# Optimization experiments

Measured on AMD Instinct MI355X. Metric: run time of the kernel, lower is better.

Reference implementation:

```python
import jax, jax.numpy as jnp
import numpy as np

N_NODES = 50000


def gcn_conv(x, row, col, deg_inv_sqrt, W, b, num_nodes):
    # PyG GCNConv: h = x @ W; out[i] = sum_{(j->i)} norm_ji * h[j] + b
    # norm_ji = deg^{-1/2}[j] * deg^{-1/2}[i], with self-loops already in (row, col).
    h = x @ W  # [N, C_out]
    norm = deg_inv_sqrt[row] * deg_inv_sqrt[col]  # [E+N]
    msgs = h[row] * norm[:, None]  # gather + scale, [E+N, C_out]
    out = jax.ops.segment_sum(msgs, col, num_segments=num_nodes)
    return out + b


def setup_inputs() -> dict:
    key = jax.random.key(0)
    ks = jax.random.split(key, 8)
    n, e = N_NODES, 1600000
    c_in, c_hid, c_out = 128, 64, 32
    x = jax.random.normal(ks[0], (n, c_in), dtype=jnp.float32)
    edge_index = jax.random.randint(ks[1], (2, e), 0, n, dtype=jnp.int64)
    s1 = 1.0 / np.sqrt(c_in)
    s2 = 1.0 / np.sqrt(c_hid)
    W1 = jax.random.uniform(ks[2], (c_in, c_hid), jnp.float32, -s1, s1)
    b1 = jnp.zeros((c_hid,), jnp.float32)
    W2 = jax.random.uniform(ks[3], (c_hid, c_out), jnp.float32, -s2, s2)
    b2 = jnp.zeros((c_out,), jnp.float32)
    W3 = jax.random.uniform(ks[4], (c_hid, c_out), jnp.float32, -s2, s2)
    b3 = jnp.zeros((c_out,), jnp.float32)
    return {"x": x, "edge_index": edge_index, "W1": W1, "b1": b1,
            "W2": W2, "b2": b2, "W3": W3, "b3": b3}


def reference(x, edge_index, W1, b1, W2, b2, W3, b3):
    n = x.shape[0]
    # add self-loops (PyG GCNConv default add_self_loops=True)
    loop = jnp.arange(n, dtype=edge_index.dtype)
    row = jnp.concatenate([edge_index[0], loop])
    col = jnp.concatenate([edge_index[1], loop])
    # symmetric normalization: deg computed over target nodes (unit edge weights)
    deg = jax.ops.segment_sum(jnp.ones_like(col, dtype=x.dtype), col, num_segments=n)
    deg_inv_sqrt = jnp.where(deg > 0, jax.lax.rsqrt(jnp.maximum(deg, 1.0)), 0.0)
    h = jax.nn.relu(gcn_conv(x, row, col, deg_inv_sqrt, W1, b1, n))
    mu = gcn_conv(h, row, col, deg_inv_sqrt, W2, b2, n)
    logvar = gcn_conv(h, row, col, deg_inv_sqrt, W3, b3, n)
    return (mu, logvar)
```

## Files before the change

kernel.cpp:

```cpp
#include <hip/hip_runtime.h>


#define NBMAX 256
#define NT2 256
#define SLOT 128
#define CAPSH 14
#define CAP (1 << CAPSH)

__device__ __forceinline__ ushort f2bf(float x) {
    unsigned u = __float_as_uint(x);
    u = (u + 0x7FFFu + ((u >> 16) & 1u)) >> 16;
    return (ushort)u;
}
__device__ __forceinline__ float bflo(unsigned u) { return __uint_as_float(u << 16); }
__device__ __forceinline__ float bfhi(unsigned u) { return __uint_as_float(u & 0xFFFF0000u); }

__device__ __forceinline__ void acc8(float* a, uint4 x) {
    a[0] += bflo(x.x); a[1] += bfhi(x.x);
    a[2] += bflo(x.y); a[3] += bfhi(x.y);
    a[4] += bflo(x.z); a[5] += bfhi(x.z);
    a[6] += bflo(x.w); a[7] += bfhi(x.w);
}

__global__ __launch_bounds__(256) void k_tilesort(const int* __restrict__ row,
                                                  const int* __restrict__ col,
                                                  int* __restrict__ binbuf,
                                                  unsigned char* __restrict__ cnt,
                                                  int e, int chunk) {
    __shared__ int lh[NBMAX];
    int tile = blockIdx.x;
    int t0 = tile * chunk;
    int t1 = t0 + chunk < e ? t0 + chunk : e;
    for (int i = threadIdx.x; i < NBMAX; i += 256) lh[i] = 0;
    __syncthreads();
    for (int i = t0 + threadIdx.x; i < t1; i += 256) {
        int c = col[i];
        int b = c >> 8;
        int pos = atomicAdd(&lh[b], 1);
        if (pos < SLOT)
            binbuf[(((b << 8) + tile) << 7) + pos] = row[i] | ((c & 255) << 16);
    }
    __syncthreads();
    for (int b = threadIdx.x; b < NBMAX; b += 256) {
        int c = lh[b];
        cnt[(tile << 8) + b] = (unsigned char)(c < SLOT ? c : SLOT);
    }
}

__global__ __launch_bounds__(256) void k_build(const int* __restrict__ binbuf,
                                               const unsigned char* __restrict__ cnt,
                                               float* __restrict__ dis,
                                               int* __restrict__ rp2,
                                               ushort* __restrict__ csr, int n) {
    __shared__ int lcnt[256], s[256], cur[256];
    int b = blockIdx.x;
    int t = threadIdx.x;
    int myc = cnt[(t << 8) + b];
    int mybase = ((b << 8) + t) << 7;
    lcnt[t] = 0;
    __syncthreads();
    for (int i = 0; i < myc; ++i) {
        int p = binbuf[mybase + i];
        atomicAdd(&lcnt[(p >> 16) & 255], 1);
    }
    __syncthreads();
    int v = lcnt[t];
    s[t] = v;
    __syncthreads();
    for (int off = 1; off < 256; off <<= 1) {
        int u = (t >= off) ? s[t - off] : 0;
        __syncthreads();
        s[t] += u;
        __syncthreads();
    }
    int node0 = b << 8;
    int nloc = n - node0 < 256 ? n - node0 : 256;
    int lo = b << CAPSH;
    if (t < nloc) {
        int beg = lo + s[t] - v;
        rp2[2 * (node0 + t)] = beg;
        rp2[2 * (node0 + t) + 1] = beg + v;
        cur[t] = beg;
        dis[node0 + t] = rsqrtf((float)v + 1.0f);
    }
    __syncthreads();
    for (int i = 0; i < myc; ++i) {
        int p = binbuf[mybase + i];
        int pos = atomicAdd(&cur[(p >> 16) & 255], 1);
        csr[pos] = (ushort)(p & 0xffff);
    }
}

__global__ __launch_bounds__(256) void k_gemm1(const float* __restrict__ x,
                                               const float* __restrict__ W,
                                               const float* __restrict__ dis,
                                               ushort* __restrict__ hs1b, int n) {
    __shared__ float4 w4[32][64];
    __shared__ float4 xs[4][16][8];
    for (int i = threadIdx.x; i < 128 * 64; i += 256) {
        int k = i >> 6, c = i & 63;
        ((float*)&w4[k >> 2][c])[k & 3] = W[i];
    }
    int wid = threadIdx.x >> 6;
    int lane = threadIdx.x & 63;
    int r0 = blockIdx.x * 64 + wid * 16;
    const float4* x4 = (const float4*)x;
    float acc[16];
#pragma unroll
    for (int r = 0; r < 16; ++r) acc[r] = 0.f;
    __syncthreads();
#pragma unroll
    for (int st = 0; st < 4; ++st) {
#pragma unroll
        for (int j = 0; j < 2; ++j) {
            int idx = j * 64 + lane;
            int rr = r0 + (idx >> 3);
            if (rr >= n) rr = n - 1;
            xs[wid][idx >> 3][idx & 7] = x4[(size_t)rr * 32 + st * 8 + (idx & 7)];
        }
#pragma unroll 2
        for (int k4 = 0; k4 < 8; ++k4) {
            float4 wv = w4[st * 8 + k4][lane];
#pragma unroll
            for (int r = 0; r < 16; ++r) {
                float4 xv = xs[wid][r][k4];
                acc[r] = fmaf(xv.x, wv.x, acc[r]);
                acc[r] = fmaf(xv.y, wv.y, acc[r]);
                acc[r] = fmaf(xv.z, wv.z, acc[r]);
                acc[r] = fmaf(xv.w, wv.w, acc[r]);
            }
        }
    }
    ushort* hb = hs1b + (size_t)(lane >> 5) * n * 32 + (lane & 31);
#pragma unroll
    for (int r = 0; r < 16; ++r) {
        int rw = r0 + r;
        if (rw < n) hb[(size_t)rw * 32] = f2bf(dis[rw] * acc[r]);
    }
}

__global__ __launch_bounds__(256) void k_pull1(const int* __restrict__ rp2,
                                               const ushort* __restrict__ csr,
                                               const ushort* __restrict__ hs1b,
                                               const float* __restrict__ dis,
                                               const float* __restrict__ b1,
                                               ushort* __restrict__ hs2b, int n) {
    int xcd = blockIdx.x & 7;
    int sid = xcd >> 2;
    int idx = (blockIdx.x >> 3) * 4 + (xcd & 3);
    int node = idx * 64 + (threadIdx.x >> 2);
    int c4 = threadIdx.x & 3;
    if (node >= n) return;
    size_t slab = (size_t)sid * n * 32;
    const uint4* h4 = (const uint4*)(hs1b + slab);
    int2 be = ((const int2*)rp2)[node];
    float a[8], b[8];
    uint4 v = h4[(size_t)node * 4 + c4];
    a[0] = bflo(v.x); a[1] = bfhi(v.x); a[2] = bflo(v.y); a[3] = bfhi(v.y);
    a[4] = bflo(v.z); a[5] = bfhi(v.z); a[6] = bflo(v.w); a[7] = bfhi(v.w);
#pragma unroll
    for (int j = 0; j < 8; ++j) b[j] = 0.f;
    int k = be.x;
    for (; k + 8 <= be.y; k += 8) {
        uint4 v0 = h4[(size_t)csr[k] * 4 + c4];
        uint4 v1 = h4[(size_t)csr[k + 1] * 4 + c4];
        uint4 v2 = h4[(size_t)csr[k + 2] * 4 + c4];
        uint4 v3 = h4[(size_t)csr[k + 3] * 4 + c4];
        uint4 v4 = h4[(size_t)csr[k + 4] * 4 + c4];
        uint4 v5 = h4[(size_t)csr[k + 5] * 4 + c4];
        uint4 v6 = h4[(size_t)csr[k + 6] * 4 + c4];
        uint4 v7 = h4[(size_t)csr[k + 7] * 4 + c4];
        acc8(a, v0); acc8(b, v1); acc8(a, v2); acc8(b, v3);
        acc8(a, v4); acc8(b, v5); acc8(a, v6); acc8(b, v7);
    }
    if (k + 4 <= be.y) {
        uint4 v0 = h4[(size_t)csr[k] * 4 + c4];
        uint4 v1 = h4[(size_t)csr[k + 1] * 4 + c4];
        uint4 v2 = h4[(size_t)csr[k + 2] * 4 + c4];
        uint4 v3 = h4[(size_t)csr[k + 3] * 4 + c4];
        acc8(a, v0); acc8(b, v1); acc8(a, v2); acc8(b, v3);
        k += 4;
    }
    for (; k < be.y; ++k) acc8(a, h4[(size_t)csr[k] * 4 + c4]);
    float d = dis[node];
    const float* b1s = b1 + sid * 32;
    float4 bb0 = *(const float4*)(b1s + c4 * 8);
    float4 bb1 = *(const float4*)(b1s + c4 * 8 + 4);
    float bj[8] = {bb0.x, bb0.y, bb0.z, bb0.w, bb1.x, bb1.y, bb1.z, bb1.w};
    float o[8];
#pragma unroll
    for (int j = 0; j < 8; ++j) {
        float tt = fmaf(d, a[j] + b[j], bj[j]);
        o[j] = tt > 0.f ? d * tt : 0.f;
    }
    uint4 w;
    w.x = (unsigned)f2bf(o[0]) | ((unsigned)f2bf(o[1]) << 16);
    w.y = (unsigned)f2bf(o[2]) | ((unsigned)f2bf(o[3]) << 16);
    w.z = (unsigned)f2bf(o[4]) | ((unsigned)f2bf(o[5]) << 16);
    w.w = (unsigned)f2bf(o[6]) | ((unsigned)f2bf(o[7]) << 16);
    ((uint4*)(hs2b + slab))[(size_t)node * 4 + c4] = w;
}

__global__ __launch_bounds__(256) void k_pull2(const int* __restrict__ rp2,
                                               const ushort* __restrict__ csr,
                                               const ushort* __restrict__ hs2b,
                                               const float* __restrict__ dis,
                                               float* __restrict__ gagg, int n) {
    int xcd = blockIdx.x & 7;
    int sid = xcd >> 2;
    int idx = (blockIdx.x >> 3) * 4 + (xcd & 3);
    int node = idx * 64 + (threadIdx.x >> 2);
    int c4 = threadIdx.x & 3;
    if (node >= n) return;
    const uint4* h4 = (const uint4*)(hs2b + (size_t)sid * n * 32);
    int2 be = ((const int2*)rp2)[node];
    float a[8], b[8];
    uint4 v = h4[(size_t)node * 4 + c4];
    a[0] = bflo(v.x); a[1] = bfhi(v.x); a[2] = bflo(v.y); a[3] = bfhi(v.y);
    a[4] = bflo(v.z); a[5] = bfhi(v.z); a[6] = bflo(v.w); a[7] = bfhi(v.w);
#pragma unroll
    for (int j = 0; j < 8; ++j) b[j] = 0.f;
    int k = be.x;
    for (; k + 8 <= be.y; k += 8) {
        uint4 v0 = h4[(size_t)csr[k] * 4 + c4];
        uint4 v1 = h4[(size_t)csr[k + 1] * 4 + c4];
        uint4 v2 = h4[(size_t)csr[k + 2] * 4 + c4];
        uint4 v3 = h4[(size_t)csr[k + 3] * 4 + c4];
        uint4 v4 = h4[(size_t)csr[k + 4] * 4 + c4];
        uint4 v5 = h4[(size_t)csr[k + 5] * 4 + c4];
        uint4 v6 = h4[(size_t)csr[k + 6] * 4 + c4];
        uint4 v7 = h4[(size_t)csr[k + 7] * 4 + c4];
        acc8(a, v0); acc8(b, v1); acc8(a, v2); acc8(b, v3);
        acc8(a, v4); acc8(b, v5); acc8(a, v6); acc8(b, v7);
    }
    if (k + 4 <= be.y) {
        uint4 v0 = h4[(size_t)csr[k] * 4 + c4];
        uint4 v1 = h4[(size_t)csr[k + 1] * 4 + c4];
        uint4 v2 = h4[(size_t)csr[k + 2] * 4 + c4];
        uint4 v3 = h4[(size_t)csr[k + 3] * 4 + c4];
        acc8(a, v0); acc8(b, v1); acc8(a, v2); acc8(b, v3);
        k += 4;
    }
    for (; k < be.y; ++k) acc8(a, h4[(size_t)csr[k] * 4 + c4]);
    float d = dis[node];
    float* dst = gagg + (size_t)node * 64 + sid * 32 + c4 * 8;
    *(float4*)dst = make_float4(d * (a[0] + b[0]), d * (a[1] + b[1]),
                                d * (a[2] + b[2]), d * (a[3] + b[3]));
    *(float4*)(dst + 4) = make_float4(d * (a[4] + b[4]), d * (a[5] + b[5]),
                                      d * (a[6] + b[6]), d * (a[7] + b[7]));
}

__global__ __launch_bounds__(256) void k_gemm23(const float* __restrict__ g,
                                                const float* __restrict__ W2,
                                                const float* __restrict__ b2,
                                                const float* __restrict__ W3,
                                                const float* __restrict__ b3,
                                                float* __restrict__ out, int n) {
    __shared__ float ws[2 * 32 * 17 * 4];
    __shared__ float4 gs[4][16 * 16];
    for (int i = threadIdx.x; i < 64 * 32; i += 256) {
        int k = i >> 5, c = i & 31;
        int a = (c * 17 + (k >> 2)) * 4 + (k & 3);
        ws[a] = W2[i];
        ws[2176 + a] = W3[i];
    }
    int wid = threadIdx.x >> 6;
    int lane = threadIdx.x & 63;
    int half = lane >> 5;
    int ch = lane & 31;
    int r0 = blockIdx.x * 64 + wid * 16;
    const float4* g4 = (const float4*)g;
#pragma unroll
    for (int j = 0; j < 4; ++j) {
        int idx = j * 64 + lane;
        int rr = r0 + (idx >> 4);
        if (rr >= n) rr = n - 1;
        gs[wid][idx] = g4[(size_t)rr * 16 + (idx & 15)];
    }
    __syncthreads();
    float acc[16];
#pragma unroll
    for (int r = 0; r < 16; ++r) acc[r] = 0.f;
    const float4* wl = (const float4*)ws;
    const float4* gw = gs[wid];
#pragma unroll 2
    for (int k4 = 0; k4 < 16; ++k4) {
        float4 wv = wl[half * 544 + ch * 17 + k4];
#pragma unroll
        for (int r = 0; r < 16; ++r) {
            float4 gv = gw[r * 16 + k4];
            acc[r] = fmaf(gv.x, wv.x, acc[r]);
            acc[r] = fmaf(gv.y, wv.y, acc[r]);
            acc[r] = fmaf(gv.z, wv.z, acc[r]);
            acc[r] = fmaf(gv.w, wv.w, acc[r]);
        }
    }
    float bb = half ? b3[ch] : b2[ch];
    size_t obase = half ? (size_t)n * 32 : 0;
#pragma unroll
    for (int r = 0; r < 16; ++r) {
        int rw = r0 + r;
        if (rw < n) out[obase + (size_t)rw * 32 + ch] = acc[r] + bb;
    }
}

extern "C" void kernel_launch(void* const* d_in, const int* in_sizes, int n_in,
                              void* d_out, int out_size, void* d_ws, size_t ws_size,
                              hipStream_t stream) {
    const float* x  = (const float*)d_in[0];
    const int*   ei = (const int*)d_in[1];
    const float* W1 = (const float*)d_in[2];
    const float* b1 = (const float*)d_in[3];
    const float* W2 = (const float*)d_in[4];
    const float* b2 = (const float*)d_in[5];
    const float* W3 = (const float*)d_in[6];
    const float* b3 = (const float*)d_in[7];

    int n = in_sizes[0] / 128;
    int e = in_sizes[1] / 2;
    int nb = (n + 255) >> 8;
    const int* row = ei;
    const int* col = ei + e;

    float* fws   = (float*)d_ws;
    float* dis   = fws;
    ushort* hs1b = (ushort*)(fws + n);
    ushort* hs2b = hs1b + (size_t)2 * n * 32;
    int* rp2     = (int*)(hs2b + (size_t)2 * n * 32);
    ushort* csr  = (ushort*)(rp2 + 2 * (size_t)n);
    float* gagg  = (float*)(csr + (size_t)nb * CAP);
    int* binbuf  = (int*)(gagg + (size_t)n * 64);
    unsigned char* cnt = (unsigned char*)(binbuf + (size_t)nb * NT2 * SLOT);
    float* out   = (float*)d_out;

    int chunk = (e + NT2 - 1) / NT2;
    int pg = (n + 63) / 64;
    int pgrid = 8 * ((pg + 3) / 4);

    dim3 blk(256);
    k_tilesort<<<NT2, blk, 0, stream>>>(row, col, binbuf, cnt, e, chunk);
    k_build<<<nb, blk, 0, stream>>>(binbuf, cnt, dis, rp2, csr, n);
    k_gemm1<<<(n + 63) / 64, blk, 0, stream>>>(x, W1, dis, hs1b, n);
    k_pull1<<<pgrid, blk, 0, stream>>>(rp2, csr, hs1b, dis, b1, hs2b, n);
    k_pull2<<<pgrid, blk, 0, stream>>>(rp2, csr, hs2b, dis, gagg, n);
    k_gemm23<<<(n + 63) / 64, blk, 0, stream>>>(gagg, W2, b2, W3, b3, out, n);
}
```

Before: 138.0 us.

## Merge edge binning and first GEMM into one launch, defer degree scaling

The edge tile-sort and the x@W1 GEMM are merged into a single kernel. The first 256 blocks bin edges and the remaining blocks compute the unscaled bf16 GEMM output, so the two independent stages run concurrently and one launch is removed. Because the GEMM no longer waits for degrees, the deg^-1/2 scaling moves into the build kernel, which rescales its 256-node slice of hs1b in place. This adds an extra read-modify-write pass over hs1b and a second bf16 rounding, and it uses a larger shared-memory footprint for the binning blocks.

```diff
diff --git a/kernel.cpp b/kernel.cpp
--- a/kernel.cpp
+++ b/kernel.cpp
@@ -22,28 +22,82 @@
     a[6] += bflo(x.w); a[7] += bfhi(x.w);
 }
 
-__global__ __launch_bounds__(256) void k_tilesort(const int* __restrict__ row,
-                                                  const int* __restrict__ col,
-                                                  int* __restrict__ binbuf,
-                                                  unsigned char* __restrict__ cnt,
-                                                  int e, int chunk) {
-    __shared__ int lh[NBMAX];
-    int tile = blockIdx.x;
-    int t0 = tile * chunk;
-    int t1 = t0 + chunk < e ? t0 + chunk : e;
-    for (int i = threadIdx.x; i < NBMAX; i += 256) lh[i] = 0;
-    __syncthreads();
-    for (int i = t0 + threadIdx.x; i < t1; i += 256) {
-        int c = col[i];
-        int b = c >> 8;
-        int pos = atomicAdd(&lh[b], 1);
-        if (pos < SLOT)
-            binbuf[(((b << 8) + tile) << 7) + pos] = row[i] | ((c & 255) << 16);
-    }
-    __syncthreads();
-    for (int b = threadIdx.x; b < NBMAX; b += 256) {
-        int c = lh[b];
-        cnt[(tile << 8) + b] = (unsigned char)(c < SLOT ? c : SLOT);
+__device__ __forceinline__ unsigned sc2(unsigned u, float d) {
+    return (unsigned)f2bf(d * bflo(u)) | ((unsigned)f2bf(d * bfhi(u)) << 16);
+}
+
+__global__ __launch_bounds__(256) void k_front(const int* __restrict__ row,
+                                               const int* __restrict__ col,
+                                               const float* __restrict__ x,
+                                               const float* __restrict__ W1,
+                                               int* __restrict__ binbuf,
+                                               unsigned char* __restrict__ cnt,
+                                               ushort* __restrict__ hs1b,
+                                               int n, int e, int chunk) {
+    __shared__ __align__(16) unsigned char smem[40960];
+    int t = threadIdx.x;
+    if (blockIdx.x < NT2) {
+        int* lh = (int*)smem;
+        int tile = blockIdx.x;
+        int t0 = tile * chunk;
+        int t1 = t0 + chunk < e ? t0 + chunk : e;
+        for (int i = t; i < NBMAX; i += 256) lh[i] = 0;
+        __syncthreads();
+        for (int i = t0 + t; i < t1; i += 256) {
+            int c = col[i];
+            int b = c >> 8;
+            int pos = atomicAdd(&lh[b], 1);
+            if (pos < SLOT)
+                binbuf[(((b << 8) + tile) << 7) + pos] = row[i] | ((c & 255) << 16);
+        }
+        __syncthreads();
+        for (int b = t; b < NBMAX; b += 256) {
+            int c = lh[b];
+            cnt[(tile << 8) + b] = (unsigned char)(c < SLOT ? c : SLOT);
+        }
+    } else {
+        float4 (*w4)[64] = reinterpret_cast<float4(*)[64]>(smem);
+        float4 (*xs)[16][8] = reinterpret_cast<float4(*)[16][8]>(smem + 32768);
+        for (int i = t; i < 128 * 64; i += 256) {
+            int k = i >> 6, c = i & 63;
+            ((float*)&w4[k >> 2][c])[k & 3] = W1[i];
+        }
+        int wid = t >> 6;
+        int lane = t & 63;
+        int r0 = (blockIdx.x - NT2) * 64 + wid * 16;
+        const float4* x4 = (const float4*)x;
+        float acc[16];
+#pragma unroll
+        for (int r = 0; r < 16; ++r) acc[r] = 0.f;
+        __syncthreads();
+#pragma unroll
+        for (int st = 0; st < 4; ++st) {
+#pragma unroll
+            for (int j = 0; j < 2; ++j) {
+                int idx = j * 64 + lane;
+                int rr = r0 + (idx >> 3);
+                if (rr >= n) rr = n - 1;
+                xs[wid][idx >> 3][idx & 7] = x4[(size_t)rr * 32 + st * 8 + (idx & 7)];
+            }
+#pragma unroll 2
+            for (int k4 = 0; k4 < 8; ++k4) {
+                float4 wv = w4[st * 8 + k4][lane];
+#pragma unroll
+                for (int r = 0; r < 16; ++r) {
+                    float4 xv = xs[wid][r][k4];
+                    acc[r] = fmaf(xv.x, wv.x, acc[r]);
+                    acc[r] = fmaf(xv.y, wv.y, acc[r]);
+                    acc[r] = fmaf(xv.z, wv.z, acc[r]);
+                    acc[r] = fmaf(xv.w, wv.w, acc[r]);
+                }
+            }
+        }
+        ushort* hb = hs1b + (size_t)(lane >> 5) * n * 32 + (lane & 31);
+#pragma unroll
+        for (int r = 0; r < 16; ++r) {
+            int rw = r0 + r;
+            if (rw < n) hb[(size_t)rw * 32] = f2bf(acc[r]);
+        }
     }
 }
 
@@ -51,8 +105,10 @@
                                                const unsigned char* __restrict__ cnt,
                                                float* __restrict__ dis,
                                                int* __restrict__ rp2,
-                                               ushort* __restrict__ csr, int n) {
+                                               ushort* __restrict__ csr,
+                                               ushort* __restrict__ hs1b, int n) {
     __shared__ int lcnt[256], s[256], cur[256];
+    __shared__ float sdis[256];
     int b = blockIdx.x;
     int t = threadIdx.x;
     int myc = cnt[(t << 8) + b];
@@ -81,7 +137,9 @@
         rp2[2 * (node0 + t)] = beg;
         rp2[2 * (node0 + t) + 1] = beg + v;
         cur[t] = beg;
-        dis[node0 + t] = rsqrtf((float)v + 1.0f);
+        float dv = rsqrtf((float)v + 1.0f);
+        dis[node0 + t] = dv;
+        sdis[t] = dv;
     }
     __syncthreads();
     for (int i = 0; i < myc; ++i) {
@@ -89,53 +147,17 @@
         int pos = atomicAdd(&cur[(p >> 16) & 255], 1);
         csr[pos] = (ushort)(p & 0xffff);
     }
-}
-
-__global__ __launch_bounds__(256) void k_gemm1(const float* __restrict__ x,
-                                               const float* __restrict__ W,
-                                               const float* __restrict__ dis,
-                                               ushort* __restrict__ hs1b, int n) {
-    __shared__ float4 w4[32][64];
-    __shared__ float4 xs[4][16][8];
-    for (int i = threadIdx.x; i < 128 * 64; i += 256) {
-        int k = i >> 6, c = i & 63;
-        ((float*)&w4[k >> 2][c])[k & 3] = W[i];
-    }
-    int wid = threadIdx.x >> 6;
-    int lane = threadIdx.x & 63;
-    int r0 = blockIdx.x * 64 + wid * 16;
-    const float4* x4 = (const float4*)x;
-    float acc[16];
-#pragma unroll
-    for (int r = 0; r < 16; ++r) acc[r] = 0.f;
-    __syncthreads();
-#pragma unroll
-    for (int st = 0; st < 4; ++st) {
-#pragma unroll
-        for (int j = 0; j < 2; ++j) {
-            int idx = j * 64 + lane;
-            int rr = r0 + (idx >> 3);
-            if (rr >= n) rr = n - 1;
-            xs[wid][idx >> 3][idx & 7] = x4[(size_t)rr * 32 + st * 8 + (idx & 7)];
-        }
-#pragma unroll 2
-        for (int k4 = 0; k4 < 8; ++k4) {
-            float4 wv = w4[st * 8 + k4][lane];
-#pragma unroll
-            for (int r = 0; r < 16; ++r) {
-                float4 xv = xs[wid][r][k4];
-                acc[r] = fmaf(xv.x, wv.x, acc[r]);
-                acc[r] = fmaf(xv.y, wv.y, acc[r]);
-                acc[r] = fmaf(xv.z, wv.z, acc[r]);
-                acc[r] = fmaf(xv.w, wv.w, acc[r]);
-            }
-        }
-    }
-    ushort* hb = hs1b + (size_t)(lane >> 5) * n * 32 + (lane & 31);
-#pragma unroll
-    for (int r = 0; r < 16; ++r) {
-        int rw = r0 + r;
-        if (rw < n) hb[(size_t)rw * 32] = f2bf(dis[rw] * acc[r]);
+    uint4* s0 = (uint4*)hs1b + (size_t)node0 * 4;
+    uint4* s1 = (uint4*)hs1b + (size_t)n * 4 + (size_t)node0 * 4;
+    for (int idx = t; idx < nloc * 4; idx += 256) {
+        float dv = sdis[idx >> 2];
+        uint4 u0 = s0[idx], u1 = s1[idx];
+        u0.x = sc2(u0.x, dv); u0.y = sc2(u0.y, dv);
+        u0.z = sc2(u0.z, dv); u0.w = sc2(u0.w, dv);
+        u1.x = sc2(u1.x, dv); u1.y = sc2(u1.y, dv);
+        u1.z = sc2(u1.z, dv); u1.w = sc2(u1.w, dv);
+        s0[idx] = u0;
+        s1[idx] = u1;
     }
 }
 
@@ -334,13 +356,13 @@
     float* out   = (float*)d_out;
 
     int chunk = (e + NT2 - 1) / NT2;
-    int pg = (n + 63) / 64;
+    int ntiles = (n + 63) / 64;
+    int pg = ntiles;
     int pgrid = 8 * ((pg + 3) / 4);
 
     dim3 blk(256);
-    k_tilesort<<<NT2, blk, 0, stream>>>(row, col, binbuf, cnt, e, chunk);
-    k_build<<<nb, blk, 0, stream>>>(binbuf, cnt, dis, rp2, csr, n);
-    k_gemm1<<<(n + 63) / 64, blk, 0, stream>>>(x, W1, dis, hs1b, n);
+    k_front<<<NT2 + ntiles, blk, 0, stream>>>(row, col, x, W1, binbuf, cnt, hs1b, n, e, chunk);
+    k_build<<<nb, blk, 0, stream>>>(binbuf, cnt, dis, rp2, csr, hs1b, n);
     k_pull1<<<pgrid, blk, 0, stream>>>(rp2, csr, hs1b, dis, b1, hs2b, n);
     k_pull2<<<pgrid, blk, 0, stream>>>(rp2, csr, hs2b, dis, gagg, n);
     k_gemm23<<<(n + 63) / 64, blk, 0, stream>>>(gagg, W2, b2, W3, b3, out, n);
```

After: 128.1 us. 1.08x faster.
